# Kernel optimization log

Hardware: AMD Instinct MI355X
Metric: run time of the kernel (lower is better)

## Reference

```python
import jax, jax.numpy as jnp
import numpy as np

BATCH = 262144

def _f64_bits_msb_first(val):
    # IEEE754 double bit pattern, MSB first (equivalent to struct.pack('>d', val))
    u = int(np.frombuffer(np.float64(val).tobytes(), dtype=np.uint64)[0])
    return [float((u >> (63 - i)) & 1) for i in range(64)]

def setup_inputs() -> dict:
    key = jax.random.key(0)
    # Table T[j] = bits of 2^(j/64), shape [64 entries, 64 bits]
    table = np.array([_f64_bits_msb_first(2.0 ** (j / 64.0)) for j in range(64)],
                     dtype=np.float32)
    idx_bits = jax.random.randint(key, (BATCH, 6), 0, 2).astype(jnp.int32)
    return {"table_bits": jnp.asarray(table), "idx_bits": idx_bits}

def reference(table_bits, idx_bits):
    """Fused MUX-tree table lookup.

    Each MUXGate(sel, B, A) = sel ? B : A on binary pulses. Level k selects on
    idx_bits[..., k] (MSB first) between the lower and upper half of the
    surviving table entries, exactly reproducing the 6-level tree of 64-bit MUXes.
    """
    batch_shape = idx_bits.shape[:-1]
    # [B, 64 entries, 64 bits]
    x = jnp.broadcast_to(table_bits, batch_shape + table_bits.shape)
    for k in range(6):  # b5 (weight 32) down to b0 (weight 1)
        n = x.shape[-2] // 2
        sel = (idx_bits[..., k] > 0)[..., None, None]
        x = jnp.where(sel, x[..., n:, :], x[..., :n, :])
    return x[..., 0, :]  # [B, 64] bit pulses of 2^(idx/64)
```

## Files before the change

### kernel.cpp

```cpp
#include <hip/hip_runtime.h>


#define B_PER_BLOCK 64

__global__ __launch_bounds__(256) void
spike_lut_kernel(const float* __restrict__ table,
                 const int* __restrict__ idx_bits,
                 float4* __restrict__ out4,
                 int batch) {
    __shared__ float4 s_table[64 * 16];
    __shared__ int    s_idx[B_PER_BLOCK];

    const int tid = threadIdx.x;
    const int b0  = blockIdx.x * B_PER_BLOCK;

    const float4* t4 = (const float4*)table;
    #pragma unroll
    for (int r = 0; r < 4; ++r) {
        s_table[r * 256 + tid] = t4[r * 256 + tid];
    }

    if (tid < B_PER_BLOCK) {
        const int b = b0 + tid;
        int idx = 0;
        if (b < batch) {
            const int* p = idx_bits + (long)b * 6;
            #pragma unroll
            for (int k = 0; k < 6; ++k) {
                idx = (idx << 1) | (p[k] > 0 ? 1 : 0);
            }
        }
        s_idx[tid] = idx;
    }
    __syncthreads();

    #pragma unroll
    for (int r = 0; r < 4; ++r) {
        const int g  = r * 256 + tid;
        const int bl = g >> 4;
        const int q  = g & 15;
        const int b  = b0 + bl;
        if (b < batch) {
            out4[(long)b * 16 + q] = s_table[s_idx[bl] * 16 + q];
        }
    }
}

extern "C" void kernel_launch(void* const* d_in, const int* in_sizes, int n_in,
                              void* d_out, int out_size, void* d_ws, size_t ws_size,
                              hipStream_t stream) {
    const float* table    = (const float*)d_in[0];
    const int*   idx_bits = (const int*)d_in[1];
    float4*      out4     = (float4*)d_out;

    const int batch  = in_sizes[1] / 6;
    const int blocks = (batch + B_PER_BLOCK - 1) / B_PER_BLOCK;

    spike_lut_kernel<<<blocks, 256, 0, stream>>>(table, idx_bits, out4, batch);
}
```

Baseline: 80.70 us.

## Process 256 rows per block with coalesced staging of index bits

Each block now handles 256 batch rows instead of 64, which cuts the number of times the 16KB table is loaded into shared memory by a factor of four. Index bits are loaded coalesced into shared memory by all threads, and every thread then computes one row's index, instead of only 64 threads doing strided global reads. A fast path for full blocks drops the bounds checks. This uses more shared memory per block and launches fewer blocks.

```diff
diff --git a/kernel.cpp b/kernel.cpp
--- a/kernel.cpp
+++ b/kernel.cpp
@@ -1,7 +1,7 @@
 #include <hip/hip_runtime.h>
 
 
-#define B_PER_BLOCK 64
+#define ROWS 256
 
 __global__ __launch_bounds__(256) void
 spike_lut_kernel(const float* __restrict__ table,
@@ -9,39 +9,59 @@
                  float4* __restrict__ out4,
                  int batch) {
     __shared__ float4 s_table[64 * 16];
-    __shared__ int    s_idx[B_PER_BLOCK];
+    __shared__ int    s_raw[ROWS * 6];
+    __shared__ int    s_idx[ROWS];
 
-    const int tid = threadIdx.x;
-    const int b0  = blockIdx.x * B_PER_BLOCK;
+    const int  tid = threadIdx.x;
+    const long b0  = (long)blockIdx.x * ROWS;
+    const bool full = (b0 + ROWS) <= batch;
 
     const float4* t4 = (const float4*)table;
     #pragma unroll
-    for (int r = 0; r < 4; ++r) {
+    for (int r = 0; r < 4; ++r)
         s_table[r * 256 + tid] = t4[r * 256 + tid];
+
+    const int* src = idx_bits + b0 * 6;
+    if (full) {
+        #pragma unroll
+        for (int r = 0; r < 6; ++r)
+            s_raw[r * 256 + tid] = src[r * 256 + tid];
+    } else {
+        const long lim = ((long)batch - b0) * 6;
+        #pragma unroll
+        for (int r = 0; r < 6; ++r) {
+            const int g = r * 256 + tid;
+            s_raw[g] = (g < lim) ? src[g] : 0;
+        }
     }
+    __syncthreads();
 
-    if (tid < B_PER_BLOCK) {
-        const int b = b0 + tid;
+    {
+        const int* p = &s_raw[tid * 6];
         int idx = 0;
-        if (b < batch) {
-            const int* p = idx_bits + (long)b * 6;
-            #pragma unroll
-            for (int k = 0; k < 6; ++k) {
-                idx = (idx << 1) | (p[k] > 0 ? 1 : 0);
-            }
-        }
+        #pragma unroll
+        for (int k = 0; k < 6; ++k)
+            idx = (idx << 1) | (p[k] > 0 ? 1 : 0);
         s_idx[tid] = idx;
     }
     __syncthreads();
 
-    #pragma unroll
-    for (int r = 0; r < 4; ++r) {
-        const int g  = r * 256 + tid;
-        const int bl = g >> 4;
-        const int q  = g & 15;
-        const int b  = b0 + bl;
-        if (b < batch) {
-            out4[(long)b * 16 + q] = s_table[s_idx[bl] * 16 + q];
+    if (full) {
+        #pragma unroll
+        for (int it = 0; it < 16; ++it) {
+            const int g  = it * 256 + tid;
+            const int bl = g >> 4;
+            const int q  = g & 15;
+            out4[(b0 + bl) * 16 + q] = s_table[s_idx[bl] * 16 + q];
+        }
+    } else {
+        #pragma unroll
+        for (int it = 0; it < 16; ++it) {
+            const int g  = it * 256 + tid;
+            const int bl = g >> 4;
+            const int q  = g & 15;
+            if (b0 + bl < batch)
+                out4[(b0 + bl) * 16 + q] = s_table[s_idx[bl] * 16 + q];
         }
     }
 }
@@ -54,7 +74,7 @@
     float4*      out4     = (float4*)d_out;
 
     const int batch  = in_sizes[1] / 6;
-    const int blocks = (batch + B_PER_BLOCK - 1) / B_PER_BLOCK;
+    const int blocks = (batch + ROWS - 1) / ROWS;
 
     spike_lut_kernel<<<blocks, 256, 0, stream>>>(table, idx_bits, out4, batch);
 }
```

Measured after the change: 80.19 us. About the same (-0.6%).
